# Performance work log

Measured on AMD Instinct MI355X. Metric: run time of the kernel, lower is better.

Reference implementation:

```python
import jax, jax.numpy as jnp
import numpy as np

B, S, D, H = 4, 2048, 1024, 16
DH = D // H  # 64


def setup_inputs() -> dict:
    key = jax.random.key(0)
    ks = jax.random.split(key, 9)
    scale = 1.0 / np.sqrt(D)
    x = jax.random.normal(ks[0], (B, S, D), dtype=jnp.float32)
    # Stacked per-head projection weights, equivalent to ModuleList of Linear(D, DH)
    Wq = jax.random.uniform(ks[1], (H, D, DH), jnp.float32, -scale, scale)
    bq = jax.random.uniform(ks[2], (H, DH), jnp.float32, -scale, scale)
    Wk = jax.random.uniform(ks[3], (H, D, DH), jnp.float32, -scale, scale)
    bk = jax.random.uniform(ks[4], (H, DH), jnp.float32, -scale, scale)
    Wv = jax.random.uniform(ks[5], (H, D, DH), jnp.float32, -scale, scale)
    bv = jax.random.uniform(ks[6], (H, DH), jnp.float32, -scale, scale)
    Wo = jax.random.uniform(ks[7], (D, D), jnp.float32, -scale, scale)
    bo = jax.random.uniform(ks[8], (D,), jnp.float32, -scale, scale)
    return {"x": x, "Wq": Wq, "bq": bq, "Wk": Wk, "bk": bk,
            "Wv": Wv, "bv": bv, "Wo": Wo, "bo": bo}


def reference(x, Wq, bq, Wk, bk, Wv, bv, Wo, bo):
    # Per-head Linear projections, batched across heads: [B,S,D]x[H,D,DH] -> [B,H,S,DH]
    q = jnp.einsum('bsd,hde->bhse', x, Wq) + bq[None, :, None, :]
    k = jnp.einsum('bsd,hde->bhse', x, Wk) + bk[None, :, None, :]
    v = jnp.einsum('bsd,hde->bhse', x, Wv) + bv[None, :, None, :]
    # Scaled dot-product attention (no mask is applied in the original forward)
    scores = jnp.einsum('bhse,bhte->bhst', q, k) / jnp.sqrt(jnp.float32(DH))
    attn = jax.nn.softmax(scores, axis=-1)
    z = jnp.einsum('bhst,bhte->bhse', attn, v)  # [B,H,S,DH]
    # Concat heads on last dim (head-major order matches torch.cat over dim=-1)
    multihead = jnp.transpose(z, (0, 2, 1, 3)).reshape(B, S, D)
    return multihead @ Wo + bo
```

## Files before the change

kernel.cpp:

```cpp
#include <hip/hip_runtime.h>
#include <hip/hip_bf16.h>
#include <cstdint>
#include <cstddef>


typedef unsigned short u16;
typedef unsigned int u32;
typedef __attribute__((ext_vector_type(8))) __bf16 bf16x8;
typedef __attribute__((ext_vector_type(8))) unsigned short u16x8;
typedef __attribute__((ext_vector_type(4))) float f32x4;
typedef __attribute__((ext_vector_type(4))) unsigned int u32x4;

__device__ __forceinline__ u16 f2bf(float f) {
  union { __hip_bfloat16 h; u16 u; } c;
  c.h = __float2bfloat16(f);
  return c.u;
}
#if defined(__has_builtin)
#if __has_builtin(__builtin_amdgcn_cvt_pk_bf16_f32)
#define HAS_PK_BF16 1
#endif
#endif
__device__ __forceinline__ u32 pk2c(float a, float b) {
#ifdef HAS_PK_BF16
  return __builtin_bit_cast(u32, __builtin_amdgcn_cvt_pk_bf16_f32(a, b));
#else
  const u32 ua = __float_as_uint(a);
  const u32 ub = __float_as_uint(b);
  const u32 ra = ua + 0x7FFFu + ((ua >> 16) & 1u);
  const u32 rb = ub + 0x7FFFu + ((ub >> 16) & 1u);
  return (ra >> 16) | (rb & 0xFFFF0000u);
#endif
}
__device__ __forceinline__ float ex2(float x) {
  return __builtin_amdgcn_exp2f(x);
}

__device__ __forceinline__ void async16(const void* g, void* l) {
  __builtin_amdgcn_global_load_lds(
      (const __attribute__((address_space(1))) void*)g,
      (__attribute__((address_space(3))) void*)l, 16, 0, 0);
}

__global__ void k_pack_all(const float* __restrict__ x,
                           const float* __restrict__ Wq, const float* __restrict__ Wk,
                           const float* __restrict__ Wv,
                           const float* __restrict__ bq, const float* __restrict__ bk,
                           const float* __restrict__ bv,
                           const float* __restrict__ Wo,
                           u16* __restrict__ xb, u16* __restrict__ Wt,
                           float* __restrict__ bqkv, u16* __restrict__ Wot) {
  __shared__ __align__(16) u16 tile[64][72];
  const int bid = blockIdx.x;
  const int t = threadIdx.x;
  if (bid < 1024) {
    const float* src;
    u16* dstp;
    int rstride, n_base, d0;
    if (bid < 768) {
      const int proj = bid >> 8, h = (bid >> 4) & 15, dt = bid & 15;
      const float* Wp = (proj == 0) ? Wq : ((proj == 1) ? Wk : Wv);
      src = Wp + h * 65536 + (dt * 64) * 64;
      rstride = 64;
      n_base = proj * 1024 + h * 64;
      d0 = dt * 64;
      dstp = Wt;
    } else {
      const int tb = bid - 768, nt = tb >> 4, dt = tb & 15;
      src = Wo + (size_t)(dt * 64) * 1024 + nt * 64;
      rstride = 1024;
      n_base = nt * 64;
      d0 = dt * 64;
      dstp = Wot;
    }
    {
      const int row = t >> 2, c0 = (t & 3) * 16;
      const float* s = src + row * rstride + c0;
#pragma unroll
      for (int j = 0; j < 4; ++j) {
        const float4 v = *(const float4*)(s + j * 4);
        ushort4 o;
        o.x = f2bf(v.x); o.y = f2bf(v.y); o.z = f2bf(v.z); o.w = f2bf(v.w);
        *(ushort4*)&tile[row][c0 + j * 4] = o;
      }
    }
    __syncthreads();
    {
      const int e = t >> 2, c0 = (t & 3) * 16;
      u16 buf[16];
#pragma unroll
      for (int i = 0; i < 16; ++i) buf[i] = tile[c0 + i][e];
      u16* d = dstp + (size_t)(n_base + e) * 1024 + d0 + c0;
      *(u16x8*)d = *(const u16x8*)&buf[0];
      *(u16x8*)(d + 8) = *(const u16x8*)&buf[8];
    }
  } else if (bid < 9216) {
    const int i = ((bid - 1024) * 256 + t) * 4;
    const float4 v = *(const float4*)(x + i);
    ushort4 o;
    o.x = f2bf(v.x); o.y = f2bf(v.y); o.z = f2bf(v.z); o.w = f2bf(v.w);
    *(ushort4*)(xb + i) = o;
  } else {
    const int n = (bid - 9216) * 256 + t;
    const int proj = n >> 10, rem = n & 1023, h = rem >> 6, e = rem & 63;
    const float* bp = (proj == 0) ? bq : ((proj == 1) ? bk : bv);
    bqkv[n] = bp[h * 64 + e];
  }
}

template <int MODE>
__global__ __launch_bounds__(256)
void k_gemm(const u16* __restrict__ A, const u16* __restrict__ Bt,
            const float* __restrict__ bias, void* __restrict__ Cout, int ldc) {
  __shared__ __align__(16) u16 Alds[128 * 32];
  __shared__ __align__(16) u16 Blds[128 * 32];
  const int t = threadIdx.x;
  const int lane = t & 63;
  const int w = t >> 6;
  const int l15 = lane & 15;
  const int quad = lane >> 4;
  const int wm = w >> 1, wn = w & 1;
  const int m0 = blockIdx.y << 7;
  const int n0 = blockIdx.x << 7;

  const u16* ga0 = A + (size_t)(m0 + (t >> 2)) * 1024 + (t & 3) * 8;
  const u16* ga1 = ga0 + (size_t)64 * 1024;
  const u16* gb0 = Bt + (size_t)(n0 + (t >> 2)) * 1024 + (t & 3) * 8;
  const u16* gb1 = gb0 + (size_t)64 * 1024;
  u16* const lA0 = Alds + w * 512;
  u16* const lA1 = Alds + w * 512 + 2048;
  u16* const lB0 = Blds + w * 512;
  u16* const lB1 = Blds + w * 512 + 2048;

  f32x4 acc[4][4];
#pragma unroll
  for (int mi = 0; mi < 4; ++mi)
#pragma unroll
    for (int ni = 0; ni < 4; ++ni) acc[mi][ni] = (f32x4){0.f, 0.f, 0.f, 0.f};

  for (int k0 = 0; k0 < 1024; k0 += 32) {
    __syncthreads();
    async16(ga0, lA0); async16(ga1, lA1);
    async16(gb0, lB0); async16(gb1, lB1);
    ga0 += 32; ga1 += 32; gb0 += 32; gb1 += 32;
    __syncthreads();
    bf16x8 af[4], bfr[4];
#pragma unroll
    for (int i = 0; i < 4; ++i) {
      af[i]  = *(const bf16x8*)(Alds + (wm * 64 + i * 16 + l15) * 32 + quad * 8);
      bfr[i] = *(const bf16x8*)(Blds + (wn * 64 + i * 16 + l15) * 32 + quad * 8);
    }
#pragma unroll
    for (int mi = 0; mi < 4; ++mi)
#pragma unroll
      for (int ni = 0; ni < 4; ++ni)
        acc[mi][ni] = __builtin_amdgcn_mfma_f32_16x16x32_bf16(af[mi], bfr[ni], acc[mi][ni], 0, 0, 0);
  }

  const int row0 = m0 + wm * 64;
  const int col0 = n0 + wn * 64;
  const float qscale = (MODE == 0 && col0 < 1024) ? 0.125f * 1.4426950408889634f : 1.0f;
#pragma unroll
  for (int mi = 0; mi < 4; ++mi) {
#pragma unroll
    for (int ni = 0; ni < 4; ++ni) {
      const int col = col0 + ni * 16 + l15;
      const float bb = bias[col];
#pragma unroll
      for (int r = 0; r < 4; ++r) {
        const int row = row0 + mi * 16 + quad * 4 + r;
        const float v = (acc[mi][ni][r] + bb) * qscale;
        if (MODE == 0) ((u16*)Cout)[(size_t)row * ldc + col] = f2bf(v);
        else           ((float*)Cout)[(size_t)row * ldc + col] = v;
      }
    }
  }
}

__global__ __launch_bounds__(256)
void k_vt(const u16* __restrict__ qkv, u16* __restrict__ vtg) {
  __shared__ u16 tile[64][72];
  const int t = threadIdx.x;
  const int bh = blockIdx.y, b = bh >> 4, h = bh & 15;
  const int s0 = blockIdx.x << 6;
  {
    const int row = t >> 2, col0 = (t & 3) * 16;
    const u16* src = qkv + (size_t)(b * 2048 + s0 + row) * 3072 + 2048 + h * 64 + col0;
    const u16x8 v0 = *(const u16x8*)src;
    const u16x8 v1 = *(const u16x8*)(src + 8);
    *(u16x8*)&tile[row][col0] = v0;
    *(u16x8*)&tile[row][col0 + 8] = v1;
  }
  __syncthreads();
  {
    const int e = t >> 2, sc = (t & 3) * 16;
    u16 buf[16];
#pragma unroll
    for (int i = 0; i < 16; ++i) buf[i] = tile[sc + i][e];
    u16* dst = vtg + ((size_t)bh * 64 + e) * 2048 + s0 + sc;
    *(u16x8*)dst = *(const u16x8*)&buf[0];
    *(u16x8*)(dst + 8) = *(const u16x8*)&buf[8];
  }
}

__global__ __launch_bounds__(256)
void k_attn(const u16* __restrict__ qkv, const u16* __restrict__ vtg,
            u16* __restrict__ mh) {
  __shared__ __align__(16) u16 smem[8192];

  const int t = threadIdx.x;
  const int lane = t & 63;
  const int w = t >> 6;
  const int l15 = lane & 15;
  const int quad = lane >> 4;
  const int bh = blockIdx.x, b = bh >> 4, h = bh & 15;
  const int s0 = blockIdx.y << 7;

  const int lam0 = t >> 3;
  const int key0 = (lam0 & 3) | (((lam0 >> 2) & 3) << 3) | (((lam0 >> 4) & 1) << 2);
  const int ck = (t & 7) ^ (lam0 & 7);
  const u16* kbase = qkv + (size_t)(b * 2048 + key0) * 3072 + 1024 + h * 64 + ck * 8;
  const int ev = t >> 2;
  const int cv = (t & 3) ^ (ev & 3) ^ ((ev >> 2) & 3);
  const u16* vbase = vtg + ((size_t)bh * 64 + ev) * 2048 + cv * 8;

  const int kofs = w * 512;
  const int vofs = 2048 + w * 512;

  const int fe = (l15 & 3) ^ (l15 >> 2);

  bf16x8 aq[2][2];
#pragma unroll
  for (int g = 0; g < 2; ++g)
#pragma unroll
    for (int ks2 = 0; ks2 < 2; ++ks2)
      aq[g][ks2] = *(const bf16x8*)(qkv +
          (size_t)(b * 2048 + s0 + w * 32 + g * 16 + l15) * 3072 +
          h * 64 + ks2 * 32 + quad * 8);

  const u32x4 onesu = (u32x4){0x3F803F80u, 0x3F803F80u, 0x3F803F80u, 0x3F803F80u};
  const bf16x8 ones = __builtin_bit_cast(bf16x8, onesu);

  f32x4 o[2][4];
  f32x4 lacc[2];
#pragma unroll
  for (int g = 0; g < 2; ++g) {
    lacc[g] = (f32x4){0.f, 0.f, 0.f, 0.f};
#pragma unroll
    for (int ne = 0; ne < 4; ++ne) o[g][ne] = (f32x4){0.f, 0.f, 0.f, 0.f};
  }

  async16(kbase, smem + kofs);
  async16(vbase, smem + vofs);
  kbase += 32 * 3072;
  vbase += 32;

#pragma unroll 2
  for (int kt = 0; kt < 64; ++kt) {
    const int cur = kt & 1;
    const u16* const Kc = smem + cur * 4096;
    const u16* const Vc = Kc + 2048;
    u16* const nb = smem + (cur ^ 1) * 4096;

    __builtin_amdgcn_s_barrier();
    async16(kbase, nb + kofs);
    async16(vbase, nb + vofs);
    kbase += 32 * 3072;
    vbase += 32;
    asm volatile("s_waitcnt vmcnt(2)" ::: "memory");
    __builtin_amdgcn_s_barrier();
    __builtin_amdgcn_sched_barrier(0);

    bf16x8 kf[2][2], bvf[4];
#pragma unroll
    for (int h2 = 0; h2 < 2; ++h2) {
      const int row = h2 * 16 + l15;
      kf[h2][0] = *(const bf16x8*)(Kc + row * 64 + ((quad) ^ (l15 & 7)) * 8);
      kf[h2][1] = *(const bf16x8*)(Kc + row * 64 + ((4 + quad) ^ (l15 & 7)) * 8);
    }
#pragma unroll
    for (int ne = 0; ne < 4; ++ne) {
      const int e = ne * 16 + l15;
      bvf[ne] = *(const bf16x8*)(Vc + e * 32 + (quad ^ fe) * 8);
    }

    f32x4 st[2][2];
    __builtin_amdgcn_s_setprio(1);
#pragma unroll
    for (int h2 = 0; h2 < 2; ++h2)
#pragma unroll
      for (int g = 0; g < 2; ++g) {
        st[h2][g] = __builtin_amdgcn_mfma_f32_16x16x32_bf16(kf[h2][0], aq[g][0], (f32x4){0.f,0.f,0.f,0.f}, 0, 0, 0);
        st[h2][g] = __builtin_amdgcn_mfma_f32_16x16x32_bf16(kf[h2][1], aq[g][1], st[h2][g], 0, 0, 0);
      }
    __builtin_amdgcn_s_setprio(0);

    u32x4 pf[2];
#pragma unroll
    for (int g = 0; g < 2; ++g)
#pragma unroll
      for (int h2 = 0; h2 < 2; ++h2) {
        const float p0 = ex2(st[h2][g][0]), p1 = ex2(st[h2][g][1]);
        const float p2 = ex2(st[h2][g][2]), p3 = ex2(st[h2][g][3]);
        pf[g][h2 * 2 + 0] = pk2c(p0, p1);
        pf[g][h2 * 2 + 1] = pk2c(p2, p3);
      }

    __builtin_amdgcn_s_setprio(1);
#pragma unroll
    for (int ne = 0; ne < 4; ++ne)
#pragma unroll
      for (int g = 0; g < 2; ++g)
        o[g][ne] = __builtin_amdgcn_mfma_f32_16x16x32_bf16(
            __builtin_bit_cast(bf16x8, pf[g]), bvf[ne], o[g][ne], 0, 0, 0);
#pragma unroll
    for (int g = 0; g < 2; ++g)
      lacc[g] = __builtin_amdgcn_mfma_f32_16x16x32_bf16(
          __builtin_bit_cast(bf16x8, pf[g]), ones, lacc[g], 0, 0, 0);
    __builtin_amdgcn_s_setprio(0);
  }

#pragma unroll
  for (int g = 0; g < 2; ++g) {
#pragma unroll
    for (int r = 0; r < 4; ++r) {
      const float iv = 1.f / lacc[g][r];
      const int row = s0 + w * 32 + g * 16 + quad * 4 + r;
#pragma unroll
      for (int ne = 0; ne < 4; ++ne) {
        const int col = h * 64 + ne * 16 + l15;
        mh[(size_t)(b * 2048 + row) * 1024 + col] = f2bf(o[g][ne][r] * iv);
      }
    }
  }
}

extern "C" void kernel_launch(void* const* d_in, const int* in_sizes, int n_in,
                              void* d_out, int out_size, void* d_ws, size_t ws_size,
                              hipStream_t stream) {
  (void)in_sizes; (void)n_in; (void)out_size; (void)ws_size;
  const float* x  = (const float*)d_in[0];
  const float* Wq = (const float*)d_in[1];
  const float* bq = (const float*)d_in[2];
  const float* Wk = (const float*)d_in[3];
  const float* bk = (const float*)d_in[4];
  const float* Wv = (const float*)d_in[5];
  const float* bv = (const float*)d_in[6];
  const float* Wo = (const float*)d_in[7];
  const float* bo = (const float*)d_in[8];

  char* ws = (char*)d_ws;
  u16*   Xb   = (u16*)  (ws + 0);
  u16*   Vtg  = (u16*)  (ws + 0);
  u16*   Wt   = (u16*)  (ws + 16777216);
  float* bqkv = (float*)(ws + 23068672);
  u16*   Wot  = (u16*)  (ws + 23080960);
  u16*   QKV  = (u16*)  (ws + 25178112);
  u16*   MH   = (u16*)  (ws + 75509760);
  float* out  = (float*)d_out;

  k_pack_all <<<9228, 256, 0, stream>>>(x, Wq, Wk, Wv, bq, bk, bv, Wo,
                                        Xb, Wt, bqkv, Wot);
  k_gemm<0>  <<<dim3(24, 64), 256, 0, stream>>>(Xb, Wt, bqkv, (void*)QKV, 3072);
  k_vt       <<<dim3(32, 64), 256, 0, stream>>>(QKV, Vtg);
  k_attn     <<<dim3(64, 16), 256, 0, stream>>>(QKV, Vtg, MH);
  k_gemm<1>  <<<dim3(8, 64), 256, 0, stream>>>(MH, Wot, bo, (void*)out, 1024);
}
```

Baseline: 296.8 us.

## Load K/V MFMA fragments directly from global into registers, dropping LDS staging

The attention loop no longer stages K and V tiles through shared memory with async copies and barriers. Each wave now loads its MFMA fragments straight from global memory, double-buffering K in registers and loading V per iteration. This removes the block-level barriers and LDS traffic, but each of the four waves now fetches the same K/V data separately and V loads are not prefetched, so latency may be exposed.

```diff
diff --git a/kernel.cpp b/kernel.cpp
--- a/kernel.cpp
+++ b/kernel.cpp
@@ -206,8 +206,6 @@
 __global__ __launch_bounds__(256)
 void k_attn(const u16* __restrict__ qkv, const u16* __restrict__ vtg,
             u16* __restrict__ mh) {
-  __shared__ __align__(16) u16 smem[8192];
-
   const int t = threadIdx.x;
   const int lane = t & 63;
   const int w = t >> 6;
@@ -216,18 +214,13 @@
   const int bh = blockIdx.x, b = bh >> 4, h = bh & 15;
   const int s0 = blockIdx.y << 7;
 
-  const int lam0 = t >> 3;
-  const int key0 = (lam0 & 3) | (((lam0 >> 2) & 3) << 3) | (((lam0 >> 4) & 1) << 2);
-  const int ck = (t & 7) ^ (lam0 & 7);
-  const u16* kbase = qkv + (size_t)(b * 2048 + key0) * 3072 + 1024 + h * 64 + ck * 8;
-  const int ev = t >> 2;
-  const int cv = (t & 3) ^ (ev & 3) ^ ((ev >> 2) & 3);
-  const u16* vbase = vtg + ((size_t)bh * 64 + ev) * 2048 + cv * 8;
-
-  const int kofs = w * 512;
-  const int vofs = 2048 + w * 512;
-
-  const int fe = (l15 & 3) ^ (l15 >> 2);
+  const int key0 = (l15 >> 2) * 8 + (l15 & 3);
+  const u16* kp0 = qkv + (size_t)(b * 2048 + key0) * 3072 + 1024 + h * 64 + quad * 8;
+  const u16* kp1 = kp0 + (size_t)4 * 3072;
+  const u16* vp0 = vtg + ((size_t)bh * 64 + l15) * 2048 + quad * 8;
+  const u16* vp1 = vp0 + (size_t)16 * 2048;
+  const u16* vp2 = vp0 + (size_t)32 * 2048;
+  const u16* vp3 = vp0 + (size_t)48 * 2048;
 
   bf16x8 aq[2][2];
 #pragma unroll
@@ -250,48 +243,38 @@
     for (int ne = 0; ne < 4; ++ne) o[g][ne] = (f32x4){0.f, 0.f, 0.f, 0.f};
   }
 
-  async16(kbase, smem + kofs);
-  async16(vbase, smem + vofs);
-  kbase += 32 * 3072;
-  vbase += 32;
+  bf16x8 kfb[2][2][2];
+  kfb[0][0][0] = *(const bf16x8*)(kp0);
+  kfb[0][0][1] = *(const bf16x8*)(kp0 + 32);
+  kfb[0][1][0] = *(const bf16x8*)(kp1);
+  kfb[0][1][1] = *(const bf16x8*)(kp1 + 32);
+  kp0 += 32 * 3072; kp1 += 32 * 3072;
 
 #pragma unroll 2
   for (int kt = 0; kt < 64; ++kt) {
-    const int cur = kt & 1;
-    const u16* const Kc = smem + cur * 4096;
-    const u16* const Vc = Kc + 2048;
-    u16* const nb = smem + (cur ^ 1) * 4096;
-
-    __builtin_amdgcn_s_barrier();
-    async16(kbase, nb + kofs);
-    async16(vbase, nb + vofs);
-    kbase += 32 * 3072;
-    vbase += 32;
-    asm volatile("s_waitcnt vmcnt(2)" ::: "memory");
-    __builtin_amdgcn_s_barrier();
-    __builtin_amdgcn_sched_barrier(0);
-
-    bf16x8 kf[2][2], bvf[4];
-#pragma unroll
-    for (int h2 = 0; h2 < 2; ++h2) {
-      const int row = h2 * 16 + l15;
-      kf[h2][0] = *(const bf16x8*)(Kc + row * 64 + ((quad) ^ (l15 & 7)) * 8);
-      kf[h2][1] = *(const bf16x8*)(Kc + row * 64 + ((4 + quad) ^ (l15 & 7)) * 8);
-    }
-#pragma unroll
-    for (int ne = 0; ne < 4; ++ne) {
-      const int e = ne * 16 + l15;
-      bvf[ne] = *(const bf16x8*)(Vc + e * 32 + (quad ^ fe) * 8);
-    }
-
-    f32x4 st[2][2];
+    const int st = kt & 1, ns = st ^ 1;
+
+    bf16x8 bvf[4];
+    bvf[0] = *(const bf16x8*)(vp0);
+    bvf[1] = *(const bf16x8*)(vp1);
+    bvf[2] = *(const bf16x8*)(vp2);
+    bvf[3] = *(const bf16x8*)(vp3);
+    vp0 += 32; vp1 += 32; vp2 += 32; vp3 += 32;
+
+    kfb[ns][0][0] = *(const bf16x8*)(kp0);
+    kfb[ns][0][1] = *(const bf16x8*)(kp0 + 32);
+    kfb[ns][1][0] = *(const bf16x8*)(kp1);
+    kfb[ns][1][1] = *(const bf16x8*)(kp1 + 32);
+    kp0 += 32 * 3072; kp1 += 32 * 3072;
+
+    f32x4 stv[2][2];
     __builtin_amdgcn_s_setprio(1);
 #pragma unroll
     for (int h2 = 0; h2 < 2; ++h2)
 #pragma unroll
       for (int g = 0; g < 2; ++g) {
-        st[h2][g] = __builtin_amdgcn_mfma_f32_16x16x32_bf16(kf[h2][0], aq[g][0], (f32x4){0.f,0.f,0.f,0.f}, 0, 0, 0);
-        st[h2][g] = __builtin_amdgcn_mfma_f32_16x16x32_bf16(kf[h2][1], aq[g][1], st[h2][g], 0, 0, 0);
+        stv[h2][g] = __builtin_amdgcn_mfma_f32_16x16x32_bf16(kfb[st][h2][0], aq[g][0], (f32x4){0.f,0.f,0.f,0.f}, 0, 0, 0);
+        stv[h2][g] = __builtin_amdgcn_mfma_f32_16x16x32_bf16(kfb[st][h2][1], aq[g][1], stv[h2][g], 0, 0, 0);
       }
     __builtin_amdgcn_s_setprio(0);
 
@@ -300,8 +283,8 @@
     for (int g = 0; g < 2; ++g)
 #pragma unroll
       for (int h2 = 0; h2 < 2; ++h2) {
-        const float p0 = ex2(st[h2][g][0]), p1 = ex2(st[h2][g][1]);
-        const float p2 = ex2(st[h2][g][2]), p3 = ex2(st[h2][g][3]);
+        const float p0 = ex2(stv[h2][g][0]), p1 = ex2(stv[h2][g][1]);
+        const float p2 = ex2(stv[h2][g][2]), p3 = ex2(stv[h2][g][3]);
         pf[g][h2 * 2 + 0] = pk2c(p0, p1);
         pf[g][h2 * 2 + 1] = pk2c(p2, p3);
       }
```

Result: slower. 430.1 us (+44.9%).
